# Kernel tuning notes

Measured on AMD Instinct MI355X. Metric: run time of the kernel, lower is better.

## Reference

```python
import jax, jax.numpy as jnp
import numpy as np

N_HEADS = 16
ROPE_BASE = 10000.0


def _rope_tables(T, Dh, dtype):
    # inv_freq over even indices of head_dim, per RotaryEmbedding
    inv_freq = 1.0 / (ROPE_BASE ** (jnp.arange(0, Dh, 2, dtype=jnp.float32) / Dh))
    freqs = jnp.outer(jnp.arange(T, dtype=jnp.float32), inv_freq)  # [T, Dh/2]
    emb = jnp.concatenate([freqs, freqs], axis=-1)                  # [T, Dh]
    return emb.astype(dtype).reshape(1, 1, T, Dh), None


def _rotate_half(x):
    x1, x2 = jnp.split(x, 2, axis=-1)
    return jnp.concatenate([-x2, x1], axis=-1)


def setup_inputs() -> dict:
    key = jax.random.key(0)
    k1, k2, k3 = jax.random.split(key, 3)
    B, T, C = 2, 2048, 1024
    x = jax.random.normal(k1, (B, T, C), dtype=jnp.float32)
    w_qkv = jax.random.normal(k2, (C, 3 * C), dtype=jnp.float32) * (1.0 / np.sqrt(C))
    w_out = jax.random.normal(k3, (C, C), dtype=jnp.float32) * (1.0 / np.sqrt(C))
    return {"x": x, "w_qkv": w_qkv, "w_out": w_out}


def reference(x, w_qkv, w_out):
    B, T, C = x.shape
    H = N_HEADS
    Dh = C // H
    qkv = x @ w_qkv                                   # [B, T, 3C]
    q, k, v = jnp.split(qkv, 3, axis=-1)
    # [B, T, C] -> [B, H, T, Dh]
    def to_heads(t):
        return t.reshape(B, T, H, Dh).transpose(0, 2, 1, 3)
    q, k, v = to_heads(q), to_heads(k), to_heads(v)

    # RoPE
    emb, _ = _rope_tables(T, Dh, x.dtype)             # [1,1,T,Dh] angle table
    cos, sin = jnp.cos(emb), jnp.sin(emb)
    q = q * cos + _rotate_half(q) * sin
    k = k * cos + _rotate_half(k) * sin

    # causal SDPA (eval mode -> no dropout)
    scale = 1.0 / jnp.sqrt(jnp.asarray(Dh, dtype=x.dtype))
    scores = jnp.einsum('bhqd,bhkd->bhqk', q, k) * scale
    causal_mask = jnp.tril(jnp.ones((T, T), dtype=bool))
    scores = jnp.where(causal_mask, scores, jnp.asarray(-jnp.inf, dtype=scores.dtype))
    attn = jax.nn.softmax(scores, axis=-1)
    out = jnp.einsum('bhqk,bhkd->bhqd', attn, v)      # [B,H,T,Dh]
    out = out.transpose(0, 2, 1, 3).reshape(B, T, C)
    return out @ w_out
```

## Files before the change

### kernel.cpp

```cpp
#include <hip/hip_runtime.h>
#include <stdint.h>


typedef __attribute__((ext_vector_type(8))) __bf16 bf16x8;
typedef __attribute__((ext_vector_type(4))) __bf16 bf16x4;
typedef __attribute__((ext_vector_type(4))) float f32x4;

#define MFMA16(a, b, c) __builtin_amdgcn_mfma_f32_16x16x32_bf16((a), (b), (c), 0, 0, 0)

#define SWAIT_VM0()                                     \
    do {                                                \
        asm volatile("s_waitcnt vmcnt(0)" ::: "memory");\
        __builtin_amdgcn_sched_barrier(0);              \
    } while (0)
#define SWAIT_LGKM0()                                     \
    do {                                                  \
        asm volatile("s_waitcnt lgkmcnt(0)" ::: "memory");\
        __builtin_amdgcn_sched_barrier(0);                \
    } while (0)

__device__ __forceinline__ void gl_lds16(const void* g, void* l) {
    __builtin_amdgcn_global_load_lds(
        (const __attribute__((address_space(1))) void*)g,
        (__attribute__((address_space(3))) void*)l, 16, 0, 0);
}

__device__ __forceinline__ unsigned short f2bf(float f) {
    union { float f; unsigned u; } x; x.f = f;
    unsigned r = x.u + 0x7FFFu + ((x.u >> 16) & 1u);
    return (unsigned short)(r >> 16);
}
__device__ __forceinline__ float bf2f(unsigned short h) {
    union { unsigned u; float f; } x; x.u = ((unsigned)h) << 16;
    return x.f;
}
__device__ __forceinline__ f32x4 fmax4(f32x4 a, f32x4 b) {
    f32x4 r;
#pragma unroll
    for (int i = 0; i < 4; i++) r[i] = fmaxf(a[i], b[i]);
    return r;
}

__global__ void cast_f32_bf16(const float* __restrict__ src,
                              unsigned short* __restrict__ dst, int n4) {
    int i = blockIdx.x * 256 + threadIdx.x;
    if (i >= n4) return;
    float4 v = ((const float4*)src)[i];
    ushort4 o;
    o.x = f2bf(v.x); o.y = f2bf(v.y); o.z = f2bf(v.z); o.w = f2bf(v.w);
    ((ushort4*)dst)[i] = o;
}

__global__ void transpose_cast(const float* __restrict__ src,
                               unsigned short* __restrict__ dst, int K, int N) {
    __shared__ float tile[32][33];
    int n0 = blockIdx.x * 32, k0 = blockIdx.y * 32;
    int r = threadIdx.x >> 5, c = threadIdx.x & 31;
#pragma unroll
    for (int i = 0; i < 4; i++) {
        int kk = r + i * 8;
        tile[kk][c] = src[(size_t)(k0 + kk) * N + n0 + c];
    }
    __syncthreads();
#pragma unroll
    for (int i = 0; i < 4; i++) {
        int nn = r + i * 8;
        dst[(size_t)(n0 + nn) * K + k0 + c] = f2bf(tile[c][nn]);
    }
}

__global__ void rope_tables(float2* __restrict__ cst) {
    int idx = blockIdx.x * 256 + threadIdx.x;
    int t = idx >> 5, d = idx & 31;
    float inv = powf(10000.0f, -(float)(2 * d) / 64.0f);
    float a = (float)t * inv;
    cst[idx] = make_float2(cosf(a), sinf(a));
}

template <int MODE>
__global__ __launch_bounds__(256) void gemm_bt(
    const unsigned short* __restrict__ A,
    const unsigned short* __restrict__ Bt,
    unsigned short* __restrict__ oq,
    unsigned short* __restrict__ ok,
    unsigned short* __restrict__ ovt,
    float* __restrict__ of,
    const float2* __restrict__ cst,
    int M_, int N_, int K_) {
    __shared__ __attribute__((aligned(16))) unsigned short ldsA[128 * 64];
    __shared__ __attribute__((aligned(16))) unsigned short ldsB[128 * 64];
    const int tid = threadIdx.x;
    const int lane = tid & 63, wv = tid >> 6;
    const int wr = wv >> 1, wc = wv & 1;
    const int l15 = lane & 15, lg = lane >> 4;
    const int lrow = lane >> 3, lch = lane & 7;
    const int swz = (lch * 16) ^ (lrow << 4);
    const int m0 = blockIdx.x * 128, n0 = blockIdx.y * 128;
    const char* Ab = (const char*)A;
    const char* Bb = (const char*)Bt;
    const size_t rstride = (size_t)K_ * 2;

    f32x4 acc[4][4] = {};

    const int nkt = K_ >> 6;
    for (int kt = 0; kt < nkt; kt++) {
        if (kt) __syncthreads();
#pragma unroll
        for (int ii = 0; ii < 4; ii++) {
            int r0 = wv * 32 + ii * 8;
            gl_lds16(Ab + (size_t)(m0 + r0 + lrow) * rstride + kt * 128 + swz,
                     (char*)ldsA + r0 * 128);
            gl_lds16(Bb + (size_t)(n0 + r0 + lrow) * rstride + kt * 128 + swz,
                     (char*)ldsB + r0 * 128);
        }
        __syncthreads();
#pragma unroll
        for (int ks = 0; ks < 2; ks++) {
            const int kb = ks * 64 + lg * 16;
            bf16x8 af[4], bfr[4];
#pragma unroll
            for (int mf = 0; mf < 4; mf++) {
                int row = wr * 64 + mf * 16 + l15;
                af[mf] = *(const bf16x8*)((const char*)ldsA + row * 128 +
                                          (kb ^ ((row & 7) << 4)));
            }
#pragma unroll
            for (int nf = 0; nf < 4; nf++) {
                int row = wc * 64 + nf * 16 + l15;
                bfr[nf] = *(const bf16x8*)((const char*)ldsB + row * 128 +
                                           (kb ^ ((row & 7) << 4)));
            }
#pragma unroll
            for (int mf = 0; mf < 4; mf++)
#pragma unroll
                for (int nf = 0; nf < 4; nf++)
                    acc[mf][nf] = MFMA16(af[mf], bfr[nf], acc[mf][nf]);
        }
    }

    if (MODE == 0) {
        const int sblk = n0 >> 10;
        if (sblk == 2) {
#pragma unroll
            for (int mf = 0; mf < 4; mf++)
#pragma unroll
                for (int nf = 0; nf < 4; nf++)
#pragma unroll
                    for (int j = 0; j < 4; j++) {
                        int grow = m0 + wr * 64 + mf * 16 + lg * 4 + j;
                        int gcol = n0 + wc * 64 + nf * 16 + l15;
                        int b = grow >> 11, t = grow & 2047;
                        int c = gcol & 1023;
                        int h = c >> 6, d = c & 63;
                        int hb = b * 16 + h;
                        ovt[((size_t)hb * 64 + d) * 2048 + t] =
                            f2bf(acc[mf][nf][j]);
                    }
        } else {
            const float QSC = 0.125f * 1.44269504f;
            unsigned short* dst = (sblk == 0) ? oq : ok;
#pragma unroll
            for (int mf = 0; mf < 4; mf++)
#pragma unroll
                for (int j = 0; j < 4; j++) {
                    int grow = m0 + wr * 64 + mf * 16 + lg * 4 + j;
                    int b = grow >> 11, t = grow & 2047;
#pragma unroll
                    for (int nf = 0; nf < 2; nf++) {
                        int gcol = n0 + wc * 64 + nf * 16 + l15;
                        int c = gcol & 1023;
                        int h = c >> 6;
                        int d = nf * 16 + l15;
                        int hb = b * 16 + h;
                        float2 csv = cst[t * 32 + d];
                        float x1 = acc[mf][nf][j];
                        float x2 = acc[mf][nf + 2][j];
                        float r1 = x1 * csv.x - x2 * csv.y;
                        float r2 = x2 * csv.x + x1 * csv.y;
                        if (sblk == 0) { r1 *= QSC; r2 *= QSC; }
                        size_t base = ((size_t)hb * 2048 + t) * 64;
                        dst[base + d] = f2bf(r1);
                        dst[base + d + 32] = f2bf(r2);
                    }
                }
        }
    } else {
#pragma unroll
        for (int mf = 0; mf < 4; mf++)
#pragma unroll
            for (int nf = 0; nf < 4; nf++)
#pragma unroll
                for (int j = 0; j < 4; j++) {
                    int grow = m0 + wr * 64 + mf * 16 + lg * 4 + j;
                    int gcol = n0 + wc * 64 + nf * 16 + l15;
                    of[(size_t)grow * N_ + gcol] = acc[mf][nf][j];
                }
    }
}

__global__ __launch_bounds__(256, 2) void attn_fwd(
    const unsigned short* __restrict__ Q,
    const unsigned short* __restrict__ K,
    const unsigned short* __restrict__ Vt,
    unsigned short* __restrict__ O) {
    __shared__ __attribute__((aligned(16))) char ldsKV[4][16384];
    __shared__ __attribute__((aligned(16))) char ldsP[4][2048];
    __shared__ float ml[4][32][2];
    const int tid = threadIdx.x, lane = tid & 63, wv = tid >> 6;
    const int l15 = lane & 15, lg = lane >> 4;
    const int lrow = lane >> 3, lch = lane & 7;
    const int swz = (lch * 16) ^ (lrow << 4);

    const int wg = blockIdx.x;
    const int jt = 63 - (wg >> 5);
    const int bh = (wg & 7) * 4 + ((wg >> 3) & 3);
    const int q0 = jt * 32;
    const int nkt = (jt >> 1) + 1;
    const int lo = (wv * nkt) >> 2;
    const int hi = ((wv + 1) * nkt) >> 2;
    const int b = bh >> 4, h = bh & 15;

    const unsigned short* Qh = Q + (size_t)bh * 2048 * 64;
    const char* Kg = (const char*)(K + (size_t)bh * 2048 * 64);
    const char* Vg = (const char*)(Vt + (size_t)bh * 64 * 2048);
    char* Kb = ldsKV[wv];
    char* Vb = ldsKV[wv] + 8192;
    char* Pb = ldsP[wv];

    bf16x8 qa[2][2];
#pragma unroll
    for (int mf = 0; mf < 2; mf++)
#pragma unroll
        for (int ks = 0; ks < 2; ks++)
            qa[mf][ks] = *(const bf16x8*)(Qh + (size_t)(q0 + mf * 16 + l15) * 64 +
                                          ks * 32 + lg * 8);

    auto stage = [&](int k0) {
        const char* kg = Kg + (size_t)k0 * 128;
        const char* vg = Vg + (size_t)k0 * 2;
#pragma unroll
        for (int ii = 0; ii < 8; ii++) {
            gl_lds16(kg + (ii * 8 + lrow) * 128 + swz, Kb + ii * 1024);
            gl_lds16(vg + (size_t)(ii * 8 + lrow) * 4096 + swz, Vb + ii * 1024);
        }
    };

    f32x4 oacc[2][4] = {};
    float mi[2] = {-1e30f, -1e30f}, li[2] = {0.f, 0.f};

    if (lo < hi) {
        stage(lo * 64);
        for (int kt = lo; kt < hi; kt++) {
            const int k0 = kt * 64;
            SWAIT_VM0();
            bf16x8 kb[2][4], vb[2][4];
#pragma unroll
            for (int ks = 0; ks < 2; ks++)
#pragma unroll
                for (int nf = 0; nf < 4; nf++) {
                    int row = nf * 16 + l15;
                    kb[ks][nf] = *(const bf16x8*)(
                        Kb + row * 128 + ((ks * 64 + lg * 16) ^ ((row & 7) << 4)));
                }
#pragma unroll
            for (int ks = 0; ks < 2; ks++)
#pragma unroll
                for (int df = 0; df < 4; df++) {
                    int row = df * 16 + l15;
                    vb[ks][df] = *(const bf16x8*)(
                        Vb + row * 128 + ((ks * 64 + lg * 16) ^ ((row & 7) << 4)));
                }
            f32x4 s[2][4] = {};
#pragma unroll
            for (int ks = 0; ks < 2; ks++)
#pragma unroll
                for (int mf = 0; mf < 2; mf++)
#pragma unroll
                    for (int nf = 0; nf < 4; nf++)
                        s[mf][nf] = MFMA16(kb[ks][nf], qa[mf][ks], s[mf][nf]);
            SWAIT_LGKM0();
            if (kt + 1 < hi) stage(k0 + 64);
            const bool maskt = (kt == nkt - 1);
#pragma unroll
            for (int mf = 0; mf < 2; mf++) {
                if (maskt) {
                    int qrow = q0 + mf * 16 + l15;
#pragma unroll
                    for (int nf = 0; nf < 4; nf++)
#pragma unroll
                        for (int j = 0; j < 4; j++)
                            if (k0 + nf * 16 + lg * 4 + j > qrow)
                                s[mf][nf][j] = -1e30f;
                }
                f32x4 t01 = fmax4(s[mf][0], s[mf][1]);
                f32x4 t23 = fmax4(s[mf][2], s[mf][3]);
                f32x4 tm = fmax4(t01, t23);
                float rmax = fmaxf(fmaxf(tm[0], tm[1]), fmaxf(tm[2], tm[3]));
                rmax = fmaxf(rmax, __shfl_xor(rmax, 16));
                rmax = fmaxf(rmax, __shfl_xor(rmax, 32));
                const float mnew = fmaxf(mi[mf], rmax);
                const float alpha = exp2f(mi[mf] - mnew);
                mi[mf] = mnew;
                float rsum = 0.f;
#pragma unroll
                for (int nf = 0; nf < 4; nf++)
#pragma unroll
                    for (int j = 0; j < 4; j++) {
                        float p = exp2f(s[mf][nf][j] - mnew);
                        s[mf][nf][j] = p;
                        rsum += p;
                    }
                rsum += __shfl_xor(rsum, 16);
                rsum += __shfl_xor(rsum, 32);
                li[mf] = li[mf] * alpha + rsum;
#pragma unroll
                for (int j = 0; j < 4; j++) {
                    float aj = __shfl(alpha, lg * 4 + j);
#pragma unroll
                    for (int df = 0; df < 4; df++) oacc[mf][df][j] *= aj;
                }
            }
#pragma unroll
            for (int ksh = 0; ksh < 2; ksh++) {
#pragma unroll
                for (int mf = 0; mf < 2; mf++) {
                    int row = mf * 16 + l15;
#pragma unroll
                    for (int nf2 = 0; nf2 < 2; nf2++) {
                        bf16x4 pk;
#pragma unroll
                        for (int j = 0; j < 4; j++)
                            pk[j] = (__bf16)s[mf][ksh * 2 + nf2][j];
                        *(bf16x4*)(Pb + row * 64 +
                                   ((nf2 * 32 + lg * 8) ^ ((row & 3) << 4))) = pk;
                    }
                }
                bf16x8 pa[2];
#pragma unroll
                for (int mf = 0; mf < 2; mf++) {
                    int row = mf * 16 + l15;
                    pa[mf] = *(const bf16x8*)(
                        Pb + row * 64 + ((lg * 16) ^ ((row & 3) << 4)));
                }
#pragma unroll
                for (int mf = 0; mf < 2; mf++)
#pragma unroll
                    for (int df = 0; df < 4; df++)
                        oacc[mf][df] = MFMA16(pa[mf], vb[ksh][df], oacc[mf][df]);
            }
        }
    }

    float* part = (float*)ldsKV[wv];
#pragma unroll
    for (int mf = 0; mf < 2; mf++)
#pragma unroll
        for (int df = 0; df < 4; df++)
#pragma unroll
            for (int j = 0; j < 4; j++)
                part[(mf * 16 + lg * 4 + j) * 68 + df * 16 + l15] =
                    oacc[mf][df][j];
    if (lg == 0) {
#pragma unroll
        for (int mf = 0; mf < 2; mf++) {
            ml[wv][mf * 16 + l15][0] = mi[mf];
            ml[wv][mf * 16 + l15][1] = li[mf];
        }
    }
    __syncthreads();
#pragma unroll
    for (int rr = 0; rr < 8; rr++) {
        const int row = wv * 8 + rr;
        float m01 = fmaxf(ml[0][row][0], ml[1][row][0]);
        float m23 = fmaxf(ml[2][row][0], ml[3][row][0]);
        float m = fmaxf(m01, m23);
        float ssum = 0.f, ov = 0.f;
#pragma unroll
        for (int v = 0; v < 4; v++) {
            float sv = exp2f(ml[v][row][0] - m);
            ssum += ml[v][row][1] * sv;
            ov += ((const float*)ldsKV[v])[row * 68 + lane] * sv;
        }
        O[((size_t)(b * 2048 + q0 + row)) * 1024 + h * 64 + lane] =
            f2bf(ov / ssum);
    }
}

extern "C" void kernel_launch(void* const* d_in, const int* in_sizes, int n_in,
                              void* d_out, int out_size, void* d_ws, size_t ws_size,
                              hipStream_t stream) {
    const float* x     = (const float*)d_in[0];
    const float* w_qkv = (const float*)d_in[1];
    const float* w_out = (const float*)d_in[2];
    float* out = (float*)d_out;
    char* ws = (char*)d_ws;
    const size_t MB = 1024 * 1024;

    unsigned short* xb    = (unsigned short*)(ws);
    unsigned short* wqkvt = (unsigned short*)(ws + 8 * MB);
    unsigned short* woutt = (unsigned short*)(ws + 14 * MB);
    unsigned short* qh    = (unsigned short*)(ws + 16 * MB);
    unsigned short* kh    = (unsigned short*)(ws + 24 * MB);
    unsigned short* vt    = (unsigned short*)(ws + 32 * MB);
    unsigned short* ao    = (unsigned short*)(ws + 40 * MB);
    float2* cst = (float2*)(ws + 48 * MB);

    cast_f32_bf16<<<4096, 256, 0, stream>>>(x, xb, (4096 * 1024) / 4);
    transpose_cast<<<dim3(96, 32), 256, 0, stream>>>(w_qkv, wqkvt, 1024, 3072);
    transpose_cast<<<dim3(32, 32), 256, 0, stream>>>(w_out, woutt, 1024, 1024);
    rope_tables<<<256, 256, 0, stream>>>(cst);

    gemm_bt<0><<<dim3(32, 24), 256, 0, stream>>>(xb, wqkvt, qh, kh, vt, nullptr,
                                                 cst, 4096, 3072, 1024);
    attn_fwd<<<2048, 256, 0, stream>>>(qh, kh, vt, ao);
    gemm_bt<1><<<dim3(32, 8), 256, 0, stream>>>(ao, woutt, nullptr, nullptr,
                                                nullptr, out, nullptr,
                                                4096, 1024, 1024);
}
```

Before: 137.8 us.

## Load V directly to registers, shrink LDS, add lazy softmax rescale and setprio

The attention kernel stops staging V through LDS and loads V fragments from global memory straight into registers, one tile ahead, which shrinks per-wave LDS so launch bounds can go from 2 to 3 blocks per CU. The online softmax skips the max reduction and accumulator rescale unless some row max rises by more than 8 (in log2 units). The P buffer is repacked as one 64-wide tile, and s_setprio is raised around the MFMA blocks. The aim is higher occupancy and less exp/shuffle work, at the cost of more register pressure and uncoalesced direct V loads. The lazy rescale lets the unnormalised exponentials grow up to 2^8, which may cost some precision.

```diff
diff --git a/kernel.cpp b/kernel.cpp
--- a/kernel.cpp
+++ b/kernel.cpp
@@ -198,13 +198,12 @@
     }
 }
 
-__global__ __launch_bounds__(256, 2) void attn_fwd(
+__global__ __launch_bounds__(256, 3) void attn_fwd(
     const unsigned short* __restrict__ Q,
     const unsigned short* __restrict__ K,
     const unsigned short* __restrict__ Vt,
     unsigned short* __restrict__ O) {
-    __shared__ __attribute__((aligned(16))) char ldsKV[4][16384];
-    __shared__ __attribute__((aligned(16))) char ldsP[4][2048];
+    __shared__ __attribute__((aligned(16))) char lds[4][12288];
     __shared__ float ml[4][32][2];
     const int tid = threadIdx.x, lane = tid & 63, wv = tid >> 6;
     const int l15 = lane & 15, lg = lane >> 4;
@@ -222,10 +221,9 @@
 
     const unsigned short* Qh = Q + (size_t)bh * 2048 * 64;
     const char* Kg = (const char*)(K + (size_t)bh * 2048 * 64);
-    const char* Vg = (const char*)(Vt + (size_t)bh * 64 * 2048);
-    char* Kb = ldsKV[wv];
-    char* Vb = ldsKV[wv] + 8192;
-    char* Pb = ldsP[wv];
+    const unsigned short* Vh = Vt + (size_t)bh * 64 * 2048;
+    char* Kb = lds[wv];
+    char* Pb = lds[wv] + 8192;
 
     bf16x8 qa[2][2];
 #pragma unroll
@@ -235,25 +233,33 @@
             qa[mf][ks] = *(const bf16x8*)(Qh + (size_t)(q0 + mf * 16 + l15) * 64 +
                                           ks * 32 + lg * 8);
 
-    auto stage = [&](int k0) {
+    auto stageK = [&](int k0) {
         const char* kg = Kg + (size_t)k0 * 128;
-        const char* vg = Vg + (size_t)k0 * 2;
-#pragma unroll
-        for (int ii = 0; ii < 8; ii++) {
+#pragma unroll
+        for (int ii = 0; ii < 8; ii++)
             gl_lds16(kg + (ii * 8 + lrow) * 128 + swz, Kb + ii * 1024);
-            gl_lds16(vg + (size_t)(ii * 8 + lrow) * 4096 + swz, Vb + ii * 1024);
-        }
     };
 
     f32x4 oacc[2][4] = {};
     float mi[2] = {-1e30f, -1e30f}, li[2] = {0.f, 0.f};
+    bf16x8 vb[2][4];
+
+#define LOADV(K0)                                                             \
+    do {                                                                      \
+        _Pragma("unroll") for (int ks = 0; ks < 2; ks++)                      \
+            _Pragma("unroll") for (int df = 0; df < 4; df++)                  \
+                vb[ks][df] = *(const bf16x8*)(                                \
+                    Vh + (size_t)(df * 16 + l15) * 2048 + (K0) + ks * 32 +    \
+                    lg * 8);                                                  \
+    } while (0)
 
     if (lo < hi) {
-        stage(lo * 64);
+        stageK(lo * 64);
+        LOADV(lo * 64);
         for (int kt = lo; kt < hi; kt++) {
             const int k0 = kt * 64;
             SWAIT_VM0();
-            bf16x8 kb[2][4], vb[2][4];
+            bf16x8 kb[2][4];
 #pragma unroll
             for (int ks = 0; ks < 2; ks++)
 #pragma unroll
@@ -262,15 +268,8 @@
                     kb[ks][nf] = *(const bf16x8*)(
                         Kb + row * 128 + ((ks * 64 + lg * 16) ^ ((row & 7) << 4)));
                 }
-#pragma unroll
-            for (int ks = 0; ks < 2; ks++)
-#pragma unroll
-                for (int df = 0; df < 4; df++) {
-                    int row = df * 16 + l15;
-                    vb[ks][df] = *(const bf16x8*)(
-                        Vb + row * 128 + ((ks * 64 + lg * 16) ^ ((row & 7) << 4)));
-                }
             f32x4 s[2][4] = {};
+            __builtin_amdgcn_s_setprio(1);
 #pragma unroll
             for (int ks = 0; ks < 2; ks++)
 #pragma unroll
@@ -278,8 +277,9 @@
 #pragma unroll
                     for (int nf = 0; nf < 4; nf++)
                         s[mf][nf] = MFMA16(kb[ks][nf], qa[mf][ks], s[mf][nf]);
+            __builtin_amdgcn_s_setprio(0);
             SWAIT_LGKM0();
-            if (kt + 1 < hi) stage(k0 + 64);
+            if (kt + 1 < hi) stageK(k0 + 64);
             const bool maskt = (kt == nkt - 1);
 #pragma unroll
             for (int mf = 0; mf < 2; mf++) {
@@ -296,62 +296,65 @@
                 f32x4 t23 = fmax4(s[mf][2], s[mf][3]);
                 f32x4 tm = fmax4(t01, t23);
                 float rmax = fmaxf(fmaxf(tm[0], tm[1]), fmaxf(tm[2], tm[3]));
-                rmax = fmaxf(rmax, __shfl_xor(rmax, 16));
-                rmax = fmaxf(rmax, __shfl_xor(rmax, 32));
-                const float mnew = fmaxf(mi[mf], rmax);
-                const float alpha = exp2f(mi[mf] - mnew);
-                mi[mf] = mnew;
+                if (__any(rmax > mi[mf] + 8.0f)) {
+                    rmax = fmaxf(rmax, __shfl_xor(rmax, 16));
+                    rmax = fmaxf(rmax, __shfl_xor(rmax, 32));
+                    float mnew = fmaxf(mi[mf], rmax);
+                    float alpha = exp2f(mi[mf] - mnew);
+                    mi[mf] = mnew;
+                    li[mf] *= alpha;
+#pragma unroll
+                    for (int j = 0; j < 4; j++) {
+                        float aj = __shfl(alpha, lg * 4 + j);
+#pragma unroll
+                        for (int df = 0; df < 4; df++) oacc[mf][df][j] *= aj;
+                    }
+                }
                 float rsum = 0.f;
 #pragma unroll
                 for (int nf = 0; nf < 4; nf++)
 #pragma unroll
                     for (int j = 0; j < 4; j++) {
-                        float p = exp2f(s[mf][nf][j] - mnew);
+                        float p = exp2f(s[mf][nf][j] - mi[mf]);
                         s[mf][nf][j] = p;
                         rsum += p;
                     }
                 rsum += __shfl_xor(rsum, 16);
                 rsum += __shfl_xor(rsum, 32);
-                li[mf] = li[mf] * alpha + rsum;
-#pragma unroll
-                for (int j = 0; j < 4; j++) {
-                    float aj = __shfl(alpha, lg * 4 + j);
-#pragma unroll
-                    for (int df = 0; df < 4; df++) oacc[mf][df][j] *= aj;
+                li[mf] += rsum;
+#pragma unroll
+                for (int nf = 0; nf < 4; nf++) {
+                    bf16x4 pk;
+#pragma unroll
+                    for (int j = 0; j < 4; j++) pk[j] = (__bf16)s[mf][nf][j];
+                    int row = mf * 16 + l15;
+                    *(bf16x4*)(Pb + row * 128 +
+                               ((nf * 32 + lg * 8) ^ ((row & 7) << 4))) = pk;
                 }
             }
 #pragma unroll
-            for (int ksh = 0; ksh < 2; ksh++) {
-#pragma unroll
-                for (int mf = 0; mf < 2; mf++) {
-                    int row = mf * 16 + l15;
-#pragma unroll
-                    for (int nf2 = 0; nf2 < 2; nf2++) {
-                        bf16x4 pk;
-#pragma unroll
-                        for (int j = 0; j < 4; j++)
-                            pk[j] = (__bf16)s[mf][ksh * 2 + nf2][j];
-                        *(bf16x4*)(Pb + row * 64 +
-                                   ((nf2 * 32 + lg * 8) ^ ((row & 3) << 4))) = pk;
-                    }
-                }
+            for (int ks = 0; ks < 2; ks++) {
                 bf16x8 pa[2];
 #pragma unroll
                 for (int mf = 0; mf < 2; mf++) {
                     int row = mf * 16 + l15;
                     pa[mf] = *(const bf16x8*)(
-                        Pb + row * 64 + ((lg * 16) ^ ((row & 3) << 4)));
-                }
+                        Pb + row * 128 + ((ks * 64 + lg * 16) ^ ((row & 7) << 4)));
+                }
+                __builtin_amdgcn_s_setprio(1);
 #pragma unroll
                 for (int mf = 0; mf < 2; mf++)
 #pragma unroll
                     for (int df = 0; df < 4; df++)
-                        oacc[mf][df] = MFMA16(pa[mf], vb[ksh][df], oacc[mf][df]);
+                        oacc[mf][df] = MFMA16(pa[mf], vb[ks][df], oacc[mf][df]);
+                __builtin_amdgcn_s_setprio(0);
             }
-        }
-    }
-
-    float* part = (float*)ldsKV[wv];
+            if (kt + 1 < hi) LOADV(k0 + 64);
+        }
+    }
+#undef LOADV
+
+    float* part = (float*)lds[wv];
 #pragma unroll
     for (int mf = 0; mf < 2; mf++)
 #pragma unroll
@@ -379,7 +382,7 @@
         for (int v = 0; v < 4; v++) {
             float sv = exp2f(ml[v][row][0] - m);
             ssum += ml[v][row][1] * sv;
-            ov += ((const float*)ldsKV[v])[row * 68 + lane] * sv;
+            ov += ((const float*)lds[v])[row * 68 + lane] * sv;
         }
         O[((size_t)(b * 2048 + q0 + row)) * 1024 + h * 64 + lane] =
             f2bf(ov / ssum);
```

Result: slower. 184.8 us (+34.1%).
